# Kernel optimization log

Measured on AMD Instinct MI355X. Metric: run time of the kernel, lower is better.

The kernel has to match this reference:

```python
import jax, jax.numpy as jnp
import numpy as np

N = 100000        # nodes
E = 1600000       # edges (avg degree 16)
D_NODE = 32
D_EDGE = 16
H = 64
C = 5


def setup_inputs() -> dict:
    key = jax.random.key(0)
    ks = jax.random.split(key, 11)
    x = jax.random.normal(ks[0], (N, D_NODE), jnp.float32)
    edge_index = jax.random.randint(ks[1], (2, E), 0, N, jnp.int32)
    edge_attr = jax.random.normal(ks[2], (E, D_EDGE), jnp.float32)
    W1 = jax.random.normal(ks[3], (D_NODE, H), jnp.float32) / np.sqrt(D_NODE)
    b1 = jax.random.normal(ks[4], (H,), jnp.float32) * 0.02
    W2 = jax.random.normal(ks[5], (H, H), jnp.float32) / np.sqrt(H)
    b2 = jax.random.normal(ks[6], (H,), jnp.float32) * 0.02
    Wc1 = jax.random.normal(ks[7], (2 * H + D_EDGE, 64), jnp.float32) / np.sqrt(2 * H + D_EDGE)
    bc1 = jax.random.normal(ks[8], (64,), jnp.float32) * 0.02
    Wc2 = jax.random.normal(ks[9], (64, C), jnp.float32) / np.sqrt(64)
    bc2 = jax.random.normal(ks[10], (C,), jnp.float32) * 0.02
    return {"x": x, "edge_index": edge_index, "edge_attr": edge_attr,
            "W1": W1, "b1": b1, "W2": W2, "b2": b2,
            "Wc1": Wc1, "bc1": bc1, "Wc2": Wc2, "bc2": bc2}


def gcn_conv(x, W, b, src, dst, n):
    h = x @ W                                   # [n, H]
    loop = jnp.arange(n, dtype=src.dtype)
    s = jnp.concatenate([src, loop])            # self-loops appended
    d = jnp.concatenate([dst, loop])
    deg = jax.ops.segment_sum(jnp.ones_like(s, h.dtype), d, num_segments=n)
    dinv = jax.lax.rsqrt(deg)                   # deg >= 1 due to self-loops
    norm = dinv[s] * dinv[d]                    # [E+n]
    out = jax.ops.segment_sum(h[s] * norm[:, None], d, num_segments=n)
    return out + b


def reference(x, edge_index, edge_attr, W1, b1, W2, b2, Wc1, bc1, Wc2, bc2):
    src, dst = edge_index[0], edge_index[1]
    n = x.shape[0]
    h = jax.nn.relu(gcn_conv(x, W1, b1, src, dst, n))
    h = gcn_conv(h, W2, b2, src, dst, n)
    # gather-concat edge features: [E, 2H + D_EDGE]
    ef = jnp.concatenate([h[src], h[dst], edge_attr], axis=1)
    out = jax.nn.relu(ef @ Wc1 + bc1) @ Wc2 + bc2
    return out
```

## Files before the change

kernel.cpp:

```cpp
#include <hip/hip_runtime.h>
#include <hip/hip_bf16.h>


typedef __attribute__((ext_vector_type(8))) short  bf16x8;
typedef __attribute__((ext_vector_type(16))) float f32x16;

__device__ inline short f2bf(float f)
{
    union { float f; unsigned u; } v; v.f = f;
    unsigned r = v.u + 0x7fff + ((v.u >> 16) & 1);
    return (short)(r >> 16);
}

__device__ inline float2 bfp2f(unsigned u)
{
    union { unsigned u; float f; } a, b;
    a.u = u << 16;
    b.u = u & 0xffff0000u;
    return make_float2(a.f, b.f);
}

__device__ inline unsigned packbf2(float a, float b)
{
    return (unsigned)(unsigned short)f2bf(a) | ((unsigned)(unsigned short)f2bf(b) << 16);
}

__global__ __launch_bounds__(256) void k_bcount(const int* __restrict__ ei, int* __restrict__ bcnt, int E)
{
    __shared__ int h[512];
    for (int i = threadIdx.x; i < 512; i += 256) h[i] = 0;
    __syncthreads();
    for (long e = (long)blockIdx.x * 256 + threadIdx.x; e < E; e += (long)gridDim.x * 256)
        atomicAdd(&h[ei[E + e] >> 8], 1);
    __syncthreads();
    for (int i = threadIdx.x; i < 512; i += 256)
        if (h[i]) atomicAdd(&bcnt[i], h[i]);
}

__global__ __launch_bounds__(512) void k_bscan(const int* __restrict__ bcnt, int nbk, int* __restrict__ bstart)
{
    __shared__ int s[512];
    int t = threadIdx.x;
    int v = (t < nbk) ? bcnt[t] : 0;
    s[t] = v;
    __syncthreads();
    for (int o = 1; o < 512; o <<= 1) {
        int a = (t >= o) ? s[t - o] : 0;
        __syncthreads();
        s[t] += a;
        __syncthreads();
    }
    if (t < nbk) bstart[t + 1] = s[t];
    if (t == 0) bstart[0] = 0;
}

__global__ __launch_bounds__(256) void k_binscatter(const int* __restrict__ ei, const int* __restrict__ bstart,
                                                    int* __restrict__ bcur, int2* __restrict__ ebs, int E)
{
    __shared__ int cnt[512], gb[512];
    const int tid = threadIdx.x;
    for (int i = tid; i < 512; i += 256) cnt[i] = 0;
    __syncthreads();
    const int base = blockIdx.x * 4096;
    int d[16], lp[16];
#pragma unroll
    for (int i = 0; i < 16; ++i) {
        int e = base + i * 256 + tid;
        if (e < E) {
            d[i] = ei[E + e];
            lp[i] = atomicAdd(&cnt[d[i] >> 8], 1);
        } else d[i] = -1;
    }
    __syncthreads();
    for (int i = tid; i < 512; i += 256) gb[i] = cnt[i] ? atomicAdd(&bcur[i], cnt[i]) : 0;
    __syncthreads();
#pragma unroll
    for (int i = 0; i < 16; ++i) {
        if (d[i] >= 0) {
            int e = base + i * 256 + tid;
            int b = d[i] >> 8;
            int2 p;
            p.x = ei[e];
            p.y = d[i];
            ebs[(size_t)bstart[b] + gb[b] + lp[i]] = p;
        }
    }
}

__global__ __launch_bounds__(256) void k_build(const int2* __restrict__ ebs, const int* __restrict__ bstart,
                                               int* __restrict__ rs, int* __restrict__ col,
                                               float* __restrict__ dinv,
                                               const float* __restrict__ x, unsigned short* __restrict__ xs,
                                               int N, int E)
{
    __shared__ int cnt[256], lstart[256], cnt2[256];
    const int b = blockIdx.x;
    const int base = b << 8;
    const int tid = threadIdx.x;
    cnt[tid] = 0; cnt2[tid] = 0;
    __syncthreads();
    const int s0 = bstart[b], s1 = bstart[b + 1];
    for (int i = s0 + tid; i < s1; i += 256) atomicAdd(&cnt[ebs[i].y - base], 1);
    __syncthreads();
    const int v = cnt[tid];
    lstart[tid] = v;
    __syncthreads();
    for (int o = 1; o < 256; o <<= 1) {
        int a = (tid >= o) ? lstart[tid - o] : 0;
        __syncthreads();
        lstart[tid] += a;
        __syncthreads();
    }
    const int node = base + tid;
    if (node < N) {
        rs[node] = s0 + lstart[tid] - v;
        dinv[node] = rsqrtf((float)(v + 1));
    }
    if (b == 0 && tid == 0) rs[N] = E;
    __syncthreads();
    for (int i = s0 + tid; i < s1; i += 256) {
        int2 p = ebs[i];
        int ln = p.y - base;
        int pos = atomicAdd(&cnt2[ln], 1);
        col[s0 + (lstart[ln] - cnt[ln]) + pos] = p.x;
    }
#pragma unroll
    for (int i = 0; i < 16; ++i) {
        int id = i * 256 + tid;
        int ni = id >> 4, pr = id & 15;
        int nd = base + ni;
        if (nd < N) {
            float dv = rsqrtf((float)(cnt[ni] + 1));
            float2 xv = *(const float2*)&x[(size_t)nd * 32 + pr * 2];
            *(unsigned*)(xs + (size_t)nd * 32 + pr * 2) = packbf2(xv.x * dv, xv.y * dv);
        }
    }
}

__global__ __launch_bounds__(256) void k_prep(const float* __restrict__ Wc1, const float* __restrict__ Wc2,
                                              const float* __restrict__ W2, const float* __restrict__ W1,
                                              const float* __restrict__ bc1, const float* __restrict__ b2,
                                              short* __restrict__ Wc1T, short* __restrict__ Wc2T,
                                              short* __restrict__ W1T, float* __restrict__ bcp)
{
    int t = blockIdx.x * 256 + threadIdx.x;
    if (t < 9216) {
        int j = t / 144, p = t - j * 144;
        float val;
        if (p < 64) {
            float s = 0.f;
            for (int k = 0; k < 64; ++k) s = fmaf(W2[p * 64 + k], Wc1[k * 64 + j], s);
            val = s;
        } else if (p < 128) {
            int m = p - 64;
            float s = 0.f;
            for (int k = 0; k < 64; ++k) s = fmaf(W2[m * 64 + k], Wc1[(64 + k) * 64 + j], s);
            val = s;
        } else {
            val = Wc1[p * 64 + j];
        }
        Wc1T[t] = f2bf(val);
    } else if (t < 11264) {
        int u = t - 9216;
        int rr = u / 64, p = u - rr * 64;
        int k = (p >> 1) + ((p & 1) << 5);
        Wc2T[u] = (rr < 5) ? f2bf(Wc2[k * 5 + rr]) : (short)0;
    } else if (t < 13312) {
        int u = t - 11264;
        int j = u / 32, k = u - j * 32;
        W1T[u] = f2bf(W1[k * 64 + j]);
    } else if (t < 13376) {
        int j = t - 13312;
        float s = bc1[j];
        for (int k = 0; k < 64; ++k) s = fmaf(b2[k], Wc1[k * 64 + j] + Wc1[(64 + k) * 64 + j], s);
        bcp[j] = s;
    }
}

__global__ __launch_bounds__(256) void k_ea(const float* __restrict__ ea, unsigned short* __restrict__ eabf, long n4)
{
    long id = (long)blockIdx.x * 256 + threadIdx.x;
    if (id >= n4) return;
    float4 v = *(const float4*)&ea[id * 4];
    short4 o;
    o.x = f2bf(v.x); o.y = f2bf(v.y); o.z = f2bf(v.z); o.w = f2bf(v.w);
    *(short4*)&eabf[id * 4] = o;
}

__global__ __launch_bounds__(256) void k_agg_x(const unsigned short* __restrict__ xs,
                                               const float* __restrict__ dinv,
                                               const int* __restrict__ rs, const int* __restrict__ col,
                                               unsigned short* __restrict__ xagg, int n)
{
    const int tid = threadIdx.x;
    const int l   = tid & 7;
    const int v   = blockIdx.x * 32 + (tid >> 3);
    if (v >= n) return;

    uint2 sv = *(const uint2*)(xs + (size_t)v * 32 + l * 4);
    float2 aL = bfp2f(sv.x), aH = bfp2f(sv.y);
    int i = rs[v];
    const int end = rs[v + 1];
    for (; i + 8 <= end; i += 8) {
        int c0 = col[i],     c1 = col[i + 1], c2 = col[i + 2], c3 = col[i + 3];
        int c4 = col[i + 4], c5 = col[i + 5], c6 = col[i + 6], c7 = col[i + 7];
        uint2 u0 = *(const uint2*)(xs + (size_t)c0 * 32 + l * 4);
        uint2 u1 = *(const uint2*)(xs + (size_t)c1 * 32 + l * 4);
        uint2 u2 = *(const uint2*)(xs + (size_t)c2 * 32 + l * 4);
        uint2 u3 = *(const uint2*)(xs + (size_t)c3 * 32 + l * 4);
        uint2 u4 = *(const uint2*)(xs + (size_t)c4 * 32 + l * 4);
        uint2 u5 = *(const uint2*)(xs + (size_t)c5 * 32 + l * 4);
        uint2 u6 = *(const uint2*)(xs + (size_t)c6 * 32 + l * 4);
        uint2 u7 = *(const uint2*)(xs + (size_t)c7 * 32 + l * 4);
        float2 p;
        p = bfp2f(u0.x); aL.x += p.x; aL.y += p.y; p = bfp2f(u0.y); aH.x += p.x; aH.y += p.y;
        p = bfp2f(u1.x); aL.x += p.x; aL.y += p.y; p = bfp2f(u1.y); aH.x += p.x; aH.y += p.y;
        p = bfp2f(u2.x); aL.x += p.x; aL.y += p.y; p = bfp2f(u2.y); aH.x += p.x; aH.y += p.y;
        p = bfp2f(u3.x); aL.x += p.x; aL.y += p.y; p = bfp2f(u3.y); aH.x += p.x; aH.y += p.y;
        p = bfp2f(u4.x); aL.x += p.x; aL.y += p.y; p = bfp2f(u4.y); aH.x += p.x; aH.y += p.y;
        p = bfp2f(u5.x); aL.x += p.x; aL.y += p.y; p = bfp2f(u5.y); aH.x += p.x; aH.y += p.y;
        p = bfp2f(u6.x); aL.x += p.x; aL.y += p.y; p = bfp2f(u6.y); aH.x += p.x; aH.y += p.y;
        p = bfp2f(u7.x); aL.x += p.x; aL.y += p.y; p = bfp2f(u7.y); aH.x += p.x; aH.y += p.y;
    }
    for (; i < end; ++i) {
        uint2 u = *(const uint2*)(xs + (size_t)col[i] * 32 + l * 4);
        float2 p;
        p = bfp2f(u.x); aL.x += p.x; aL.y += p.y;
        p = bfp2f(u.y); aH.x += p.x; aH.y += p.y;
    }
    const float dv = dinv[v];
    uint2 o;
    o.x = packbf2(dv * aL.x, dv * aL.y);
    o.y = packbf2(dv * aH.x, dv * aH.y);
    *(uint2*)(xagg + (size_t)v * 32 + l * 4) = o;
}

__global__ __launch_bounds__(256) void k_agg64(const unsigned short* __restrict__ hsc,
                                               const float* __restrict__ dinv,
                                               const int* __restrict__ rs, const int* __restrict__ col,
                                               unsigned short* __restrict__ out, int n)
{
    const int tid = threadIdx.x;
    const int l   = tid & 15;
    const int v   = blockIdx.x * 16 + (tid >> 4);
    if (v >= n) return;

    uint2 sv = *(const uint2*)(hsc + (size_t)v * 64 + l * 4);
    float2 aL = bfp2f(sv.x), aH = bfp2f(sv.y);
    int i = rs[v];
    const int end = rs[v + 1];
    for (; i + 8 <= end; i += 8) {
        int c0 = col[i],     c1 = col[i + 1], c2 = col[i + 2], c3 = col[i + 3];
        int c4 = col[i + 4], c5 = col[i + 5], c6 = col[i + 6], c7 = col[i + 7];
        uint2 u0 = *(const uint2*)(hsc + (size_t)c0 * 64 + l * 4);
        uint2 u1 = *(const uint2*)(hsc + (size_t)c1 * 64 + l * 4);
        uint2 u2 = *(const uint2*)(hsc + (size_t)c2 * 64 + l * 4);
        uint2 u3 = *(const uint2*)(hsc + (size_t)c3 * 64 + l * 4);
        uint2 u4 = *(const uint2*)(hsc + (size_t)c4 * 64 + l * 4);
        uint2 u5 = *(const uint2*)(hsc + (size_t)c5 * 64 + l * 4);
        uint2 u6 = *(const uint2*)(hsc + (size_t)c6 * 64 + l * 4);
        uint2 u7 = *(const uint2*)(hsc + (size_t)c7 * 64 + l * 4);
        float2 p;
        p = bfp2f(u0.x); aL.x += p.x; aL.y += p.y; p = bfp2f(u0.y); aH.x += p.x; aH.y += p.y;
        p = bfp2f(u1.x); aL.x += p.x; aL.y += p.y; p = bfp2f(u1.y); aH.x += p.x; aH.y += p.y;
        p = bfp2f(u2.x); aL.x += p.x; aL.y += p.y; p = bfp2f(u2.y); aH.x += p.x; aH.y += p.y;
        p = bfp2f(u3.x); aL.x += p.x; aL.y += p.y; p = bfp2f(u3.y); aH.x += p.x; aH.y += p.y;
        p = bfp2f(u4.x); aL.x += p.x; aL.y += p.y; p = bfp2f(u4.y); aH.x += p.x; aH.y += p.y;
        p = bfp2f(u5.x); aL.x += p.x; aL.y += p.y; p = bfp2f(u5.y); aH.x += p.x; aH.y += p.y;
        p = bfp2f(u6.x); aL.x += p.x; aL.y += p.y; p = bfp2f(u6.y); aH.x += p.x; aH.y += p.y;
        p = bfp2f(u7.x); aL.x += p.x; aL.y += p.y; p = bfp2f(u7.y); aH.x += p.x; aH.y += p.y;
    }
    for (; i < end; ++i) {
        uint2 u = *(const uint2*)(hsc + (size_t)col[i] * 64 + l * 4);
        float2 p;
        p = bfp2f(u.x); aL.x += p.x; aL.y += p.y;
        p = bfp2f(u.y); aH.x += p.x; aH.y += p.y;
    }
    const float dv = dinv[v];
    uint2 o;
    o.x = packbf2(dv * aL.x, dv * aL.y);
    o.y = packbf2(dv * aH.x, dv * aH.y);
    *(uint2*)(out + (size_t)v * 64 + l * 4) = o;
}

__global__ __launch_bounds__(256) void k_node1(const unsigned short* __restrict__ xagg,
                                               const short* __restrict__ W1T,
                                               const float* __restrict__ b1, const float* __restrict__ dinv,
                                               unsigned short* __restrict__ h1s, int n)
{
    const int tid = threadIdx.x;
    const int w = tid >> 6, lane = tid & 63, r = lane & 31, kg = lane >> 5;
    const int nb = blockIdx.x * 128 + w * 32;

    bf16x8 a0[2], a1[2];
#pragma unroll
    for (int t = 0; t < 2; ++t) {
        a0[t] = *(const bf16x8*)&W1T[r * 32 + t * 16 + kg * 8];
        a1[t] = *(const bf16x8*)&W1T[(r + 32) * 32 + t * 16 + kg * 8];
    }

    int row = nb + r;
    if (row >= n) row = n - 1;
    f32x16 acc0 = {0.f}, acc1 = {0.f};
#pragma unroll
    for (int t = 0; t < 2; ++t) {
        bf16x8 b = *(const bf16x8*)&xagg[(size_t)row * 32 + t * 16 + kg * 8];
        acc0 = __builtin_amdgcn_mfma_f32_32x32x16_bf16(a0[t], b, acc0, 0, 0, 0);
        acc1 = __builtin_amdgcn_mfma_f32_32x32x16_bf16(a1[t], b, acc1, 0, 0, 0);
    }

    const int node = nb + r;
    if (node < n) {
        const float dv = dinv[node];
#pragma unroll
        for (int q = 0; q < 4; ++q) {
            const int j0 = 8 * q + 4 * kg;
            float4 bA = *(const float4*)&b1[j0];
            float4 bB = *(const float4*)&b1[j0 + 32];
            short4 s0, s1;
            float t0, t1;
            t0 = acc0[4 * q]     + bA.x; t0 = t0 > 0.f ? t0 : 0.f; s0.x = f2bf(t0 * dv);
            t0 = acc0[4 * q + 1] + bA.y; t0 = t0 > 0.f ? t0 : 0.f; s0.y = f2bf(t0 * dv);
            t0 = acc0[4 * q + 2] + bA.z; t0 = t0 > 0.f ? t0 : 0.f; s0.z = f2bf(t0 * dv);
            t0 = acc0[4 * q + 3] + bA.w; t0 = t0 > 0.f ? t0 : 0.f; s0.w = f2bf(t0 * dv);
            t1 = acc1[4 * q]     + bB.x; t1 = t1 > 0.f ? t1 : 0.f; s1.x = f2bf(t1 * dv);
            t1 = acc1[4 * q + 1] + bB.y; t1 = t1 > 0.f ? t1 : 0.f; s1.y = f2bf(t1 * dv);
            t1 = acc1[4 * q + 2] + bB.z; t1 = t1 > 0.f ? t1 : 0.f; s1.z = f2bf(t1 * dv);
            t1 = acc1[4 * q + 3] + bB.w; t1 = t1 > 0.f ? t1 : 0.f; s1.w = f2bf(t1 * dv);
            *(short4*)&h1s[(size_t)node * 64 + j0]      = s0;
            *(short4*)&h1s[(size_t)node * 64 + j0 + 32] = s1;
        }
    }
}

template <int ABF>
__global__ __launch_bounds__(256) void k_edge_mlp_mfma(
    const unsigned short* __restrict__ zrow, const void* __restrict__ eattr,
    const int* __restrict__ ei,
    const short* __restrict__ Wc1T, const float* __restrict__ bcp,
    const short* __restrict__ Wc2T, const float* __restrict__ bc2,
    float* __restrict__ out, int E)
{
    __shared__ char slab[4 * 8192];

    const int tid = threadIdx.x;
    const int w = tid >> 6, lane = tid & 63, r = lane & 31, kg = lane >> 5;
    const int q = lane & 3, sr = lane >> 2;

    char* myslab = slab + w * 8192;

    const long eb = (long)blockIdx.x * 128 + w * 32;
    long ecl = eb + r; if (ecl >= E) ecl = E - 1;
    const int ns = ei[ecl];
    const int nd = ei[E + ecl];

    bf16x8 aa;
    if (ABF) {
        aa = *(const bf16x8*)((const unsigned short*)eattr + (size_t)ecl * 16 + kg * 8);
    } else {
        const float* arow = (const float*)eattr + (size_t)ecl * 16;
        float4 alo = *(const float4*)&arow[kg * 8];
        float4 ahi = *(const float4*)&arow[kg * 8 + 4];
        aa[0] = f2bf(alo.x); aa[1] = f2bf(alo.y); aa[2] = f2bf(alo.z); aa[3] = f2bf(alo.w);
        aa[4] = f2bf(ahi.x); aa[5] = f2bf(ahi.y); aa[6] = f2bf(ahi.z); aa[7] = f2bf(ahi.w);
    }

    {
        int n0 = __shfl(ns, sr);
        int n1 = __shfl(ns, 16 + sr);
        int m0 = __shfl(nd, sr);
        int m1 = __shfl(nd, 16 + sr);
        int4 s0 = *(const int4*)&zrow[(size_t)n0 * 64 + q * 8];
        int4 s1 = *(const int4*)&zrow[(size_t)n0 * 64 + 32 + q * 8];
        int4 s2 = *(const int4*)&zrow[(size_t)n1 * 64 + q * 8];
        int4 s3 = *(const int4*)&zrow[(size_t)n1 * 64 + 32 + q * 8];
        int4 d0 = *(const int4*)&zrow[(size_t)m0 * 64 + q * 8];
        int4 d1 = *(const int4*)&zrow[(size_t)m0 * 64 + 32 + q * 8];
        int4 d2 = *(const int4*)&zrow[(size_t)m1 * 64 + q * 8];
        int4 d3 = *(const int4*)&zrow[(size_t)m1 * 64 + 32 + q * 8];
        const int x0 = (sr ^ q) * 16, x1 = (16 + (sr ^ q)) * 16;
        *(int4*)(myslab + q * 512 + x0)              = s0;
        *(int4*)(myslab + (4 + q) * 512 + x0)        = s1;
        *(int4*)(myslab + q * 512 + x1)              = s2;
        *(int4*)(myslab + (4 + q) * 512 + x1)        = s3;
        *(int4*)(myslab + 4096 + q * 512 + x0)       = d0;
        *(int4*)(myslab + 4096 + (4 + q) * 512 + x0) = d1;
        *(int4*)(myslab + 4096 + q * 512 + x1)       = d2;
        *(int4*)(myslab + 4096 + (4 + q) * 512 + x1) = d3;
    }

    f32x16 acc0, acc1;
    const float bias0 = bcp[r], bias1 = bcp[r + 32];
#pragma unroll
    for (int i = 0; i < 16; ++i) { acc0[i] = bias0; acc1[i] = bias1; }

#pragma unroll
    for (int t = 0; t < 4; ++t) {
        const int c = 2 * t + kg;
        bf16x8 a  = *(const bf16x8*)(myslab + c * 512 + ((r ^ (c & 3)) * 16));
        bf16x8 w0 = *(const bf16x8*)&Wc1T[r * 144 + t * 16 + kg * 8];
        bf16x8 w1 = *(const bf16x8*)&Wc1T[(r + 32) * 144 + t * 16 + kg * 8];
        acc0 = __builtin_amdgcn_mfma_f32_32x32x16_bf16(a, w0, acc0, 0, 0, 0);
        acc1 = __builtin_amdgcn_mfma_f32_32x32x16_bf16(a, w1, acc1, 0, 0, 0);
    }
#pragma unroll
    for (int t = 0; t < 4; ++t) {
        const int c = 2 * t + kg;
        bf16x8 a  = *(const bf16x8*)(myslab + 4096 + c * 512 + ((r ^ (c & 3)) * 16));
        bf16x8 w0 = *(const bf16x8*)&Wc1T[r * 144 + (4 + t) * 16 + kg * 8];
        bf16x8 w1 = *(const bf16x8*)&Wc1T[(r + 32) * 144 + (4 + t) * 16 + kg * 8];
        acc0 = __builtin_amdgcn_mfma_f32_32x32x16_bf16(a, w0, acc0, 0, 0, 0);
        acc1 = __builtin_amdgcn_mfma_f32_32x32x16_bf16(a, w1, acc1, 0, 0, 0);
    }
    {
        bf16x8 w0 = *(const bf16x8*)&Wc1T[r * 144 + 128 + kg * 8];
        bf16x8 w1 = *(const bf16x8*)&Wc1T[(r + 32) * 144 + 128 + kg * 8];
        acc0 = __builtin_amdgcn_mfma_f32_32x32x16_bf16(aa, w0, acc0, 0, 0, 0);
        acc1 = __builtin_amdgcn_mfma_f32_32x32x16_bf16(aa, w1, acc1, 0, 0, 0);
    }

#pragma unroll
    for (int reg = 0; reg < 16; ++reg) {
        const int row = (reg & 3) + 8 * (reg >> 2) + 4 * kg;
        float v0 = acc0[reg]; v0 = v0 > 0.f ? v0 : 0.f;
        float v1 = acc1[reg]; v1 = v1 > 0.f ? v1 : 0.f;
        *(unsigned*)(myslab + row * 128 + ((4 * r) ^ ((row & 7) << 4))) = packbf2(v0, v1);
    }

    const float bias2 = (r < 5) ? bc2[r] : 0.f;
    f32x16 acc2;
#pragma unroll
    for (int i = 0; i < 16; ++i) acc2[i] = bias2;
#pragma unroll
    for (int t2 = 0; t2 < 4; ++t2) {
        const int m = t2 * 2 + kg;
        bf16x8 a  = *(const bf16x8*)(myslab + r * 128 + ((16 * m) ^ ((r & 7) << 4)));
        bf16x8 bw = *(const bf16x8*)&Wc2T[r * 64 + t2 * 16 + kg * 8];
        acc2 = __builtin_amdgcn_mfma_f32_32x32x16_bf16(a, bw, acc2, 0, 0, 0);
    }

#pragma unroll
    for (int reg = 0; reg < 16; ++reg) {
        const int row = (reg & 3) + 8 * (reg >> 2) + 4 * kg;
        const long eo = eb + row;
        if (r < 5 && eo < E) out[(size_t)eo * 5 + r] = acc2[reg];
    }
}

extern "C" void kernel_launch(void* const* d_in, const int* in_sizes, int n_in,
                              void* d_out, int out_size, void* d_ws, size_t ws_size,
                              hipStream_t stream)
{
    const float* x     = (const float*)d_in[0];
    const int*   ei    = (const int*)d_in[1];
    const float* eattr = (const float*)d_in[2];
    const float* W1    = (const float*)d_in[3];
    const float* b1    = (const float*)d_in[4];
    const float* W2    = (const float*)d_in[5];
    const float* b2    = (const float*)d_in[6];
    const float* Wc1   = (const float*)d_in[7];
    const float* bc1   = (const float*)d_in[8];
    const float* Wc2   = (const float*)d_in[9];
    const float* bc2   = (const float*)d_in[10];
    float* outp = (float*)d_out;

    const int N = in_sizes[0] / 32;
    const int E = in_sizes[1] / 2;
    const int nbk = (N + 255) >> 8;

    size_t off = 0;
    char* base = (char*)d_ws;
    auto carve = [&](size_t bytes) -> void* {
        void* p = base + off;
        off += (bytes + 255) & ~(size_t)255;
        return p;
    };
    int*   bcnt   = (int*)carve(1024 * 4);
    int*   bcur   = bcnt + 512;
    int*   bstart = (int*)carve(520 * 4);
    float* dinv   = (float*)carve((size_t)N * 4);
    int*   rs     = (int*)carve((size_t)(N + 1) * 4);
    int*   col    = (int*)carve((size_t)E * 4);
    int2*  ebs    = (int2*)carve((size_t)E * 8);
    unsigned short* xs    = (unsigned short*)carve((size_t)N * 32 * 2);
    unsigned short* xagg  = (unsigned short*)carve((size_t)N * 32 * 2);
    unsigned short* h1s   = (unsigned short*)carve((size_t)N * 64 * 2);
    unsigned short* xagg2 = (unsigned short*)carve((size_t)N * 64 * 2);
    short* Wc1T   = (short*)carve(9216 * 2);
    short* Wc2T   = (short*)carve(2048 * 2);
    short* W1T    = (short*)carve(2048 * 2);
    float* bcp    = (float*)carve(64 * 4);
    unsigned short* eabf = (unsigned short*)carve((size_t)E * 16 * 2);
    const bool use_abf = (off <= ws_size);
    (void)n_in; (void)out_size;

    const int NAX = (N + 31) / 32;
    const int NA  = (N + 15) / 16;
    const int NM  = (N + 127) / 128;
    const int NT  = (E + 127) / 128;
    const int NSC = (E + 4095) / 4096;

    hipMemsetAsync(bcnt, 0, 1024 * 4, stream);

    k_prep<<<68, 256, 0, stream>>>(Wc1, Wc2, W2, W1, bc1, b2, Wc1T, Wc2T, W1T, bcp);
    if (use_abf) k_ea<<<(int)(((long)E * 4 + 255) / 256), 256, 0, stream>>>(eattr, eabf, (long)E * 4);

    k_bcount<<<1024, 256, 0, stream>>>(ei, bcnt, E);
    k_bscan<<<1, 512, 0, stream>>>(bcnt, nbk, bstart);
    k_binscatter<<<NSC, 256, 0, stream>>>(ei, bstart, bcur, ebs, E);
    k_build<<<nbk, 256, 0, stream>>>(ebs, bstart, rs, col, dinv, x, xs, N, E);

    k_agg_x<<<NAX, 256, 0, stream>>>(xs, dinv, rs, col, xagg, N);
    k_node1<<<NM, 256, 0, stream>>>(xagg, W1T, b1, dinv, h1s, N);
    k_agg64<<<NA, 256, 0, stream>>>(h1s, dinv, rs, col, xagg2, N);

    if (use_abf)
        k_edge_mlp_mfma<1><<<NT, 256, 0, stream>>>(xagg2, eabf, ei, Wc1T, bcp, Wc2T, bc2, outp, E);
    else
        k_edge_mlp_mfma<0><<<NT, 256, 0, stream>>>(xagg2, eattr, ei, Wc1T, bcp, Wc2T, bc2, outp, E);
}
```

Baseline: 293.9 us.

## Fuse weight prep, histogram and edge-attr cast; fuse layer-1 aggregation with MFMA

Merges the weight-prep, destination-bucket histogram and edge-attribute bf16 conversion kernels into one launch that splits work by block index. It also fuses the first-layer neighbour aggregation with the W1 MFMA matmul. The aggregated rows are staged in LDS instead of written to and re-read from a global buffer. The aggregation now uses 2 threads per node instead of 8, which lowers gather parallelism per node and may hurt latency hiding.

```diff
diff --git a/kernel.cpp b/kernel.cpp
--- a/kernel.cpp
+++ b/kernel.cpp
@@ -25,16 +25,69 @@
     return (unsigned)(unsigned short)f2bf(a) | ((unsigned)(unsigned short)f2bf(b) << 16);
 }
 
-__global__ __launch_bounds__(256) void k_bcount(const int* __restrict__ ei, int* __restrict__ bcnt, int E)
-{
+__global__ __launch_bounds__(256) void k_prep_hist_ea(
+    const float* __restrict__ Wc1, const float* __restrict__ Wc2,
+    const float* __restrict__ W2, const float* __restrict__ W1,
+    const float* __restrict__ bc1, const float* __restrict__ b2,
+    short* __restrict__ Wc1T, short* __restrict__ Wc2T,
+    short* __restrict__ W1T, float* __restrict__ bcp,
+    const int* __restrict__ ei, int* __restrict__ bcnt,
+    const float* __restrict__ ea, unsigned short* __restrict__ eabf,
+    int E, int do_ea)
+{
+    if (blockIdx.x < 68) {
+        int t = blockIdx.x * 256 + threadIdx.x;
+        if (t < 9216) {
+            int j = t / 144, p = t - j * 144;
+            float val;
+            if (p < 64) {
+                float s = 0.f;
+                for (int k = 0; k < 64; ++k) s = fmaf(W2[p * 64 + k], Wc1[k * 64 + j], s);
+                val = s;
+            } else if (p < 128) {
+                int m = p - 64;
+                float s = 0.f;
+                for (int k = 0; k < 64; ++k) s = fmaf(W2[m * 64 + k], Wc1[(64 + k) * 64 + j], s);
+                val = s;
+            } else {
+                val = Wc1[p * 64 + j];
+            }
+            Wc1T[t] = f2bf(val);
+        } else if (t < 11264) {
+            int u = t - 9216;
+            int rr = u / 64, p = u - rr * 64;
+            int k = (p >> 1) + ((p & 1) << 5);
+            Wc2T[u] = (rr < 5) ? f2bf(Wc2[k * 5 + rr]) : (short)0;
+        } else if (t < 13312) {
+            int u = t - 11264;
+            int j = u / 32, k = u - j * 32;
+            W1T[u] = f2bf(W1[k * 64 + j]);
+        } else if (t < 13376) {
+            int j = t - 13312;
+            float s = bc1[j];
+            for (int k = 0; k < 64; ++k) s = fmaf(b2[k], Wc1[k * 64 + j] + Wc1[(64 + k) * 64 + j], s);
+            bcp[j] = s;
+        }
+        return;
+    }
+    const int bid = blockIdx.x - 68;
     __shared__ int h[512];
     for (int i = threadIdx.x; i < 512; i += 256) h[i] = 0;
     __syncthreads();
-    for (long e = (long)blockIdx.x * 256 + threadIdx.x; e < E; e += (long)gridDim.x * 256)
+    for (long e = (long)bid * 256 + threadIdx.x; e < E; e += (long)1024 * 256)
         atomicAdd(&h[ei[E + e] >> 8], 1);
     __syncthreads();
     for (int i = threadIdx.x; i < 512; i += 256)
         if (h[i]) atomicAdd(&bcnt[i], h[i]);
+    if (do_ea) {
+        const long n4 = (long)E * 4;
+        for (long id = (long)bid * 256 + threadIdx.x; id < n4; id += (long)1024 * 256) {
+            float4 v = *(const float4*)&ea[id * 4];
+            short4 o;
+            o.x = f2bf(v.x); o.y = f2bf(v.y); o.z = f2bf(v.z); o.w = f2bf(v.w);
+            *(short4*)&eabf[id * 4] = o;
+        }
+    }
 }
 
 __global__ __launch_bounds__(512) void k_bscan(const int* __restrict__ bcnt, int nbk, int* __restrict__ bstart)
@@ -137,102 +190,147 @@
     }
 }
 
-__global__ __launch_bounds__(256) void k_prep(const float* __restrict__ Wc1, const float* __restrict__ Wc2,
-                                              const float* __restrict__ W2, const float* __restrict__ W1,
-                                              const float* __restrict__ bc1, const float* __restrict__ b2,
-                                              short* __restrict__ Wc1T, short* __restrict__ Wc2T,
-                                              short* __restrict__ W1T, float* __restrict__ bcp)
-{
-    int t = blockIdx.x * 256 + threadIdx.x;
-    if (t < 9216) {
-        int j = t / 144, p = t - j * 144;
-        float val;
-        if (p < 64) {
-            float s = 0.f;
-            for (int k = 0; k < 64; ++k) s = fmaf(W2[p * 64 + k], Wc1[k * 64 + j], s);
-            val = s;
-        } else if (p < 128) {
-            int m = p - 64;
-            float s = 0.f;
-            for (int k = 0; k < 64; ++k) s = fmaf(W2[m * 64 + k], Wc1[(64 + k) * 64 + j], s);
-            val = s;
+__global__ __launch_bounds__(256) void k_aggnode1(
+    const unsigned short* __restrict__ xs, const float* __restrict__ dinv,
+    const int* __restrict__ rs, const int* __restrict__ col,
+    const short* __restrict__ W1T, const float* __restrict__ b1,
+    unsigned short* __restrict__ h1s, int n)
+{
+    __shared__ char xlds[128 * 64];
+
+    const int tid  = threadIdx.x;
+    const int nloc = tid >> 1;
+    const int half = tid & 1;
+    const int v    = blockIdx.x * 128 + nloc;
+
+    {
+        float2 A[8];
+        if (v < n) {
+            const unsigned short* row = xs + (size_t)v * 32 + half * 16;
+            uint4 u0 = *(const uint4*)row;
+            uint4 u1 = *(const uint4*)(row + 8);
+            A[0] = bfp2f(u0.x); A[1] = bfp2f(u0.y); A[2] = bfp2f(u0.z); A[3] = bfp2f(u0.w);
+            A[4] = bfp2f(u1.x); A[5] = bfp2f(u1.y); A[6] = bfp2f(u1.z); A[7] = bfp2f(u1.w);
+            int i = rs[v];
+            const int end = rs[v + 1];
+            for (; i + 4 <= end; i += 4) {
+                int c0 = col[i], c1 = col[i + 1], c2 = col[i + 2], c3 = col[i + 3];
+                uint4 g0 = *(const uint4*)(xs + (size_t)c0 * 32 + half * 16);
+                uint4 g1 = *(const uint4*)(xs + (size_t)c0 * 32 + half * 16 + 8);
+                uint4 g2 = *(const uint4*)(xs + (size_t)c1 * 32 + half * 16);
+                uint4 g3 = *(const uint4*)(xs + (size_t)c1 * 32 + half * 16 + 8);
+                uint4 g4 = *(const uint4*)(xs + (size_t)c2 * 32 + half * 16);
+                uint4 g5 = *(const uint4*)(xs + (size_t)c2 * 32 + half * 16 + 8);
+                uint4 g6 = *(const uint4*)(xs + (size_t)c3 * 32 + half * 16);
+                uint4 g7 = *(const uint4*)(xs + (size_t)c3 * 32 + half * 16 + 8);
+                float2 p;
+                p = bfp2f(g0.x); A[0].x += p.x; A[0].y += p.y;
+                p = bfp2f(g0.y); A[1].x += p.x; A[1].y += p.y;
+                p = bfp2f(g0.z); A[2].x += p.x; A[2].y += p.y;
+                p = bfp2f(g0.w); A[3].x += p.x; A[3].y += p.y;
+                p = bfp2f(g1.x); A[4].x += p.x; A[4].y += p.y;
+                p = bfp2f(g1.y); A[5].x += p.x; A[5].y += p.y;
+                p = bfp2f(g1.z); A[6].x += p.x; A[6].y += p.y;
+                p = bfp2f(g1.w); A[7].x += p.x; A[7].y += p.y;
+                p = bfp2f(g2.x); A[0].x += p.x; A[0].y += p.y;
+                p = bfp2f(g2.y); A[1].x += p.x; A[1].y += p.y;
+                p = bfp2f(g2.z); A[2].x += p.x; A[2].y += p.y;
+                p = bfp2f(g2.w); A[3].x += p.x; A[3].y += p.y;
+                p = bfp2f(g3.x); A[4].x += p.x; A[4].y += p.y;
+                p = bfp2f(g3.y); A[5].x += p.x; A[5].y += p.y;
+                p = bfp2f(g3.z); A[6].x += p.x; A[6].y += p.y;
+                p = bfp2f(g3.w); A[7].x += p.x; A[7].y += p.y;
+                p = bfp2f(g4.x); A[0].x += p.x; A[0].y += p.y;
+                p = bfp2f(g4.y); A[1].x += p.x; A[1].y += p.y;
+                p = bfp2f(g4.z); A[2].x += p.x; A[2].y += p.y;
+                p = bfp2f(g4.w); A[3].x += p.x; A[3].y += p.y;
+                p = bfp2f(g5.x); A[4].x += p.x; A[4].y += p.y;
+                p = bfp2f(g5.y); A[5].x += p.x; A[5].y += p.y;
+                p = bfp2f(g5.z); A[6].x += p.x; A[6].y += p.y;
+                p = bfp2f(g5.w); A[7].x += p.x; A[7].y += p.y;
+                p = bfp2f(g6.x); A[0].x += p.x; A[0].y += p.y;
+                p = bfp2f(g6.y); A[1].x += p.x; A[1].y += p.y;
+                p = bfp2f(g6.z); A[2].x += p.x; A[2].y += p.y;
+                p = bfp2f(g6.w); A[3].x += p.x; A[3].y += p.y;
+                p = bfp2f(g7.x); A[4].x += p.x; A[4].y += p.y;
+                p = bfp2f(g7.y); A[5].x += p.x; A[5].y += p.y;
+                p = bfp2f(g7.z); A[6].x += p.x; A[6].y += p.y;
+                p = bfp2f(g7.w); A[7].x += p.x; A[7].y += p.y;
+            }
+            for (; i < end; ++i) {
+                int c = col[i];
+                uint4 g0 = *(const uint4*)(xs + (size_t)c * 32 + half * 16);
+                uint4 g1 = *(const uint4*)(xs + (size_t)c * 32 + half * 16 + 8);
+                float2 p;
+                p = bfp2f(g0.x); A[0].x += p.x; A[0].y += p.y;
+                p = bfp2f(g0.y); A[1].x += p.x; A[1].y += p.y;
+                p = bfp2f(g0.z); A[2].x += p.x; A[2].y += p.y;
+                p = bfp2f(g0.w); A[3].x += p.x; A[3].y += p.y;
+                p = bfp2f(g1.x); A[4].x += p.x; A[4].y += p.y;
+                p = bfp2f(g1.y); A[5].x += p.x; A[5].y += p.y;
+                p = bfp2f(g1.z); A[6].x += p.x; A[6].y += p.y;
+                p = bfp2f(g1.w); A[7].x += p.x; A[7].y += p.y;
+            }
+            const float dv = dinv[v];
+            uint4 o0, o1;
+            o0.x = packbf2(dv * A[0].x, dv * A[0].y);
+            o0.y = packbf2(dv * A[1].x, dv * A[1].y);
+            o0.z = packbf2(dv * A[2].x, dv * A[2].y);
+            o0.w = packbf2(dv * A[3].x, dv * A[3].y);
+            o1.x = packbf2(dv * A[4].x, dv * A[4].y);
+            o1.y = packbf2(dv * A[5].x, dv * A[5].y);
+            o1.z = packbf2(dv * A[6].x, dv * A[6].y);
+            o1.w = packbf2(dv * A[7].x, dv * A[7].y);
+            *(uint4*)(xlds + nloc * 64 + half * 32)      = o0;
+            *(uint4*)(xlds + nloc * 64 + half * 32 + 16) = o1;
         } else {
-            val = Wc1[p * 64 + j];
+            uint4 z = {0, 0, 0, 0};
+            *(uint4*)(xlds + nloc * 64 + half * 32)      = z;
+            *(uint4*)(xlds + nloc * 64 + half * 32 + 16) = z;
         }
-        Wc1T[t] = f2bf(val);
-    } else if (t < 11264) {
-        int u = t - 9216;
-        int rr = u / 64, p = u - rr * 64;
-        int k = (p >> 1) + ((p & 1) << 5);
-        Wc2T[u] = (rr < 5) ? f2bf(Wc2[k * 5 + rr]) : (short)0;
-    } else if (t < 13312) {
-        int u = t - 11264;
-        int j = u / 32, k = u - j * 32;
-        W1T[u] = f2bf(W1[k * 64 + j]);
-    } else if (t < 13376) {
-        int j = t - 13312;
-        float s = bc1[j];
-        for (int k = 0; k < 64; ++k) s = fmaf(b2[k], Wc1[k * 64 + j] + Wc1[(64 + k) * 64 + j], s);
-        bcp[j] = s;
-    }
-}
-
-__global__ __launch_bounds__(256) void k_ea(const float* __restrict__ ea, unsigned short* __restrict__ eabf, long n4)
-{
-    long id = (long)blockIdx.x * 256 + threadIdx.x;
-    if (id >= n4) return;
-    float4 v = *(const float4*)&ea[id * 4];
-    short4 o;
-    o.x = f2bf(v.x); o.y = f2bf(v.y); o.z = f2bf(v.z); o.w = f2bf(v.w);
-    *(short4*)&eabf[id * 4] = o;
-}
-
-__global__ __launch_bounds__(256) void k_agg_x(const unsigned short* __restrict__ xs,
-                                               const float* __restrict__ dinv,
-                                               const int* __restrict__ rs, const int* __restrict__ col,
-                                               unsigned short* __restrict__ xagg, int n)
-{
-    const int tid = threadIdx.x;
-    const int l   = tid & 7;
-    const int v   = blockIdx.x * 32 + (tid >> 3);
-    if (v >= n) return;
-
-    uint2 sv = *(const uint2*)(xs + (size_t)v * 32 + l * 4);
-    float2 aL = bfp2f(sv.x), aH = bfp2f(sv.y);
-    int i = rs[v];
-    const int end = rs[v + 1];
-    for (; i + 8 <= end; i += 8) {
-        int c0 = col[i],     c1 = col[i + 1], c2 = col[i + 2], c3 = col[i + 3];
-        int c4 = col[i + 4], c5 = col[i + 5], c6 = col[i + 6], c7 = col[i + 7];
-        uint2 u0 = *(const uint2*)(xs + (size_t)c0 * 32 + l * 4);
-        uint2 u1 = *(const uint2*)(xs + (size_t)c1 * 32 + l * 4);
-        uint2 u2 = *(const uint2*)(xs + (size_t)c2 * 32 + l * 4);
-        uint2 u3 = *(const uint2*)(xs + (size_t)c3 * 32 + l * 4);
-        uint2 u4 = *(const uint2*)(xs + (size_t)c4 * 32 + l * 4);
-        uint2 u5 = *(const uint2*)(xs + (size_t)c5 * 32 + l * 4);
-        uint2 u6 = *(const uint2*)(xs + (size_t)c6 * 32 + l * 4);
-        uint2 u7 = *(const uint2*)(xs + (size_t)c7 * 32 + l * 4);
-        float2 p;
-        p = bfp2f(u0.x); aL.x += p.x; aL.y += p.y; p = bfp2f(u0.y); aH.x += p.x; aH.y += p.y;
-        p = bfp2f(u1.x); aL.x += p.x; aL.y += p.y; p = bfp2f(u1.y); aH.x += p.x; aH.y += p.y;
-        p = bfp2f(u2.x); aL.x += p.x; aL.y += p.y; p = bfp2f(u2.y); aH.x += p.x; aH.y += p.y;
-        p = bfp2f(u3.x); aL.x += p.x; aL.y += p.y; p = bfp2f(u3.y); aH.x += p.x; aH.y += p.y;
-        p = bfp2f(u4.x); aL.x += p.x; aL.y += p.y; p = bfp2f(u4.y); aH.x += p.x; aH.y += p.y;
-        p = bfp2f(u5.x); aL.x += p.x; aL.y += p.y; p = bfp2f(u5.y); aH.x += p.x; aH.y += p.y;
-        p = bfp2f(u6.x); aL.x += p.x; aL.y += p.y; p = bfp2f(u6.y); aH.x += p.x; aH.y += p.y;
-        p = bfp2f(u7.x); aL.x += p.x; aL.y += p.y; p = bfp2f(u7.y); aH.x += p.x; aH.y += p.y;
-    }
-    for (; i < end; ++i) {
-        uint2 u = *(const uint2*)(xs + (size_t)col[i] * 32 + l * 4);
-        float2 p;
-        p = bfp2f(u.x); aL.x += p.x; aL.y += p.y;
-        p = bfp2f(u.y); aH.x += p.x; aH.y += p.y;
-    }
-    const float dv = dinv[v];
-    uint2 o;
-    o.x = packbf2(dv * aL.x, dv * aL.y);
-    o.y = packbf2(dv * aH.x, dv * aH.y);
-    *(uint2*)(xagg + (size_t)v * 32 + l * 4) = o;
+    }
+    __syncthreads();
+
+    const int w = tid >> 6, lane = tid & 63, r = lane & 31, kg = lane >> 5;
+    const int nb = blockIdx.x * 128 + w * 32;
+
+    bf16x8 a0[2], a1[2];
+#pragma unroll
+    for (int t = 0; t < 2; ++t) {
+        a0[t] = *(const bf16x8*)&W1T[r * 32 + t * 16 + kg * 8];
+        a1[t] = *(const bf16x8*)&W1T[(r + 32) * 32 + t * 16 + kg * 8];
+    }
+
+    f32x16 acc0 = {0.f}, acc1 = {0.f};
+#pragma unroll
+    for (int t = 0; t < 2; ++t) {
+        bf16x8 b = *(const bf16x8*)(xlds + (w * 32 + r) * 64 + (t * 16 + kg * 8) * 2);
+        acc0 = __builtin_amdgcn_mfma_f32_32x32x16_bf16(a0[t], b, acc0, 0, 0, 0);
+        acc1 = __builtin_amdgcn_mfma_f32_32x32x16_bf16(a1[t], b, acc1, 0, 0, 0);
+    }
+
+    const int node = nb + r;
+    if (node < n) {
+        const float dv = dinv[node];
+#pragma unroll
+        for (int q = 0; q < 4; ++q) {
+            const int j0 = 8 * q + 4 * kg;
+            float4 bA = *(const float4*)&b1[j0];
+            float4 bB = *(const float4*)&b1[j0 + 32];
+            short4 s0, s1;
+            float t0, t1;
+            t0 = acc0[4 * q]     + bA.x; t0 = t0 > 0.f ? t0 : 0.f; s0.x = f2bf(t0 * dv);
+            t0 = acc0[4 * q + 1] + bA.y; t0 = t0 > 0.f ? t0 : 0.f; s0.y = f2bf(t0 * dv);
+            t0 = acc0[4 * q + 2] + bA.z; t0 = t0 > 0.f ? t0 : 0.f; s0.z = f2bf(t0 * dv);
+            t0 = acc0[4 * q + 3] + bA.w; t0 = t0 > 0.f ? t0 : 0.f; s0.w = f2bf(t0 * dv);
+            t1 = acc1[4 * q]     + bB.x; t1 = t1 > 0.f ? t1 : 0.f; s1.x = f2bf(t1 * dv);
+            t1 = acc1[4 * q + 1] + bB.y; t1 = t1 > 0.f ? t1 : 0.f; s1.y = f2bf(t1 * dv);
+            t1 = acc1[4 * q + 2] + bB.z; t1 = t1 > 0.f ? t1 : 0.f; s1.z = f2bf(t1 * dv);
+            t1 = acc1[4 * q + 3] + bB.w; t1 = t1 > 0.f ? t1 : 0.f; s1.w = f2bf(t1 * dv);
+            *(short4*)&h1s[(size_t)node * 64 + j0]      = s0;
+            *(short4*)&h1s[(size_t)node * 64 + j0 + 32] = s1;
+        }
+    }
 }
 
 __global__ __launch_bounds__(256) void k_agg64(const unsigned short* __restrict__ hsc,
@@ -283,56 +381,6 @@
     *(uint2*)(out + (size_t)v * 64 + l * 4) = o;
 }
 
-__global__ __launch_bounds__(256) void k_node1(const unsigned short* __restrict__ xagg,
-                                               const short* __restrict__ W1T,
-                                               const float* __restrict__ b1, const float* __restrict__ dinv,
-                                               unsigned short* __restrict__ h1s, int n)
-{
-    const int tid = threadIdx.x;
-    const int w = tid >> 6, lane = tid & 63, r = lane & 31, kg = lane >> 5;
-    const int nb = blockIdx.x * 128 + w * 32;
-
-    bf16x8 a0[2], a1[2];
-#pragma unroll
-    for (int t = 0; t < 2; ++t) {
-        a0[t] = *(const bf16x8*)&W1T[r * 32 + t * 16 + kg * 8];
-        a1[t] = *(const bf16x8*)&W1T[(r + 32) * 32 + t * 16 + kg * 8];
-    }
-
-    int row = nb + r;
-    if (row >= n) row = n - 1;
-    f32x16 acc0 = {0.f}, acc1 = {0.f};
-#pragma unroll
-    for (int t = 0; t < 2; ++t) {
-        bf16x8 b = *(const bf16x8*)&xagg[(size_t)row * 32 + t * 16 + kg * 8];
-        acc0 = __builtin_amdgcn_mfma_f32_32x32x16_bf16(a0[t], b, acc0, 0, 0, 0);
-        acc1 = __builtin_amdgcn_mfma_f32_32x32x16_bf16(a1[t], b, acc1, 0, 0, 0);
-    }
-
-    const int node = nb + r;
-    if (node < n) {
-        const float dv = dinv[node];
-#pragma unroll
-        for (int q = 0; q < 4; ++q) {
-            const int j0 = 8 * q + 4 * kg;
-            float4 bA = *(const float4*)&b1[j0];
-            float4 bB = *(const float4*)&b1[j0 + 32];
-            short4 s0, s1;
-            float t0, t1;
-            t0 = acc0[4 * q]     + bA.x; t0 = t0 > 0.f ? t0 : 0.f; s0.x = f2bf(t0 * dv);
-            t0 = acc0[4 * q + 1] + bA.y; t0 = t0 > 0.f ? t0 : 0.f; s0.y = f2bf(t0 * dv);
-            t0 = acc0[4 * q + 2] + bA.z; t0 = t0 > 0.f ? t0 : 0.f; s0.z = f2bf(t0 * dv);
-            t0 = acc0[4 * q + 3] + bA.w; t0 = t0 > 0.f ? t0 : 0.f; s0.w = f2bf(t0 * dv);
-            t1 = acc1[4 * q]     + bB.x; t1 = t1 > 0.f ? t1 : 0.f; s1.x = f2bf(t1 * dv);
-            t1 = acc1[4 * q + 1] + bB.y; t1 = t1 > 0.f ? t1 : 0.f; s1.y = f2bf(t1 * dv);
-            t1 = acc1[4 * q + 2] + bB.z; t1 = t1 > 0.f ? t1 : 0.f; s1.z = f2bf(t1 * dv);
-            t1 = acc1[4 * q + 3] + bB.w; t1 = t1 > 0.f ? t1 : 0.f; s1.w = f2bf(t1 * dv);
-            *(short4*)&h1s[(size_t)node * 64 + j0]      = s0;
-            *(short4*)&h1s[(size_t)node * 64 + j0 + 32] = s1;
-        }
-    }
-}
-
 template <int ABF>
 __global__ __launch_bounds__(256) void k_edge_mlp_mfma(
     const unsigned short* __restrict__ zrow, const void* __restrict__ eattr,
@@ -483,7 +531,6 @@
     int*   col    = (int*)carve((size_t)E * 4);
     int2*  ebs    = (int2*)carve((size_t)E * 8);
     unsigned short* xs    = (unsigned short*)carve((size_t)N * 32 * 2);
-    unsigned short* xagg  = (unsigned short*)carve((size_t)N * 32 * 2);
     unsigned short* h1s   = (unsigned short*)carve((size_t)N * 64 * 2);
     unsigned short* xagg2 = (unsigned short*)carve((size_t)N * 64 * 2);
     short* Wc1T   = (short*)carve(9216 * 2);
@@ -494,24 +541,21 @@
     const bool use_abf = (off <= ws_size);
     (void)n_in; (void)out_size;
 
-    const int NAX = (N + 31) / 32;
-    const int NA  = (N + 15) / 16;
-    const int NM  = (N + 127) / 128;
-    const int NT  = (E + 127) / 128;
-    const int NSC = (E + 4095) / 4096;
+    const int NAN1 = (N + 127) / 128;
+    const int NA   = (N + 15) / 16;
+    const int NT   = (E + 127) / 128;
+    const int NSC  = (E + 4095) / 4096;
 
     hipMemsetAsync(bcnt, 0, 1024 * 4, stream);
 
-    k_prep<<<68, 256, 0, stream>>>(Wc1, Wc2, W2, W1, bc1, b2, Wc1T, Wc2T, W1T, bcp);
-    if (use_abf) k_ea<<<(int)(((long)E * 4 + 255) / 256), 256, 0, stream>>>(eattr, eabf, (long)E * 4);
-
-    k_bcount<<<1024, 256, 0, stream>>>(ei, bcnt, E);
+    k_prep_hist_ea<<<68 + 1024, 256, 0, stream>>>(Wc1, Wc2, W2, W1, bc1, b2,
+                                                  Wc1T, Wc2T, W1T, bcp,
+                                                  ei, bcnt, eattr, eabf, E, use_abf ? 1 : 0);
     k_bscan<<<1, 512, 0, stream>>>(bcnt, nbk, bstart);
     k_binscatter<<<NSC, 256, 0, stream>>>(ei, bstart, bcur, ebs, E);
     k_build<<<nbk, 256, 0, stream>>>(ebs, bstart, rs, col, dinv, x, xs, N, E);
 
-    k_agg_x<<<NAX, 256, 0, stream>>>(xs, dinv, rs, col, xagg, N);
-    k_node1<<<NM, 256, 0, stream>>>(xagg, W1T, b1, dinv, h1s, N);
+    k_aggnode1<<<NAN1, 256, 0, stream>>>(xs, dinv, rs, col, W1T, b1, h1s, N);
     k_agg64<<<NA, 256, 0, stream>>>(h1s, dinv, rs, col, xagg2, N);
 
     if (use_abf)
```

Measured after the change: 284.5 us. 1.03x faster.
